# Kernel optimization log

Measured on AMD Instinct MI355X. Metric: run time of the kernel, lower is better.

The kernel has to match this reference:

```python
import jax, jax.numpy as jnp
import numpy as np

N = 100000   # nodes
E = 1600000  # edges
G = 64       # graphs in batch
DIMS = [(7, 128), (128, 128), (128, 256)]
EPS = 1e-5


def setup_inputs() -> dict:
    key = jax.random.key(0)
    ks = jax.random.split(key, 32)
    inp = {}
    inp["x"] = jax.random.normal(ks[0], (N, 7), dtype=jnp.float32)
    inp["edge_index"] = jax.random.randint(ks[1], (2, E), 0, N, dtype=jnp.int64)
    inp["batch"] = jnp.sort(jax.random.randint(ks[2], (N,), 0, G, dtype=jnp.int64))
    ki = 3
    for i, (din, dout) in enumerate(DIMS):
        inp[f"Wl{i}"] = jax.random.normal(ks[ki], (din, dout), dtype=jnp.float32) * 0.05; ki += 1
        inp[f"bl{i}"] = jnp.zeros((dout,), dtype=jnp.float32)
        inp[f"Wr{i}"] = jax.random.normal(ks[ki], (din, dout), dtype=jnp.float32) * 0.05; ki += 1
        inp[f"g{i}"] = jax.random.uniform(ks[ki], (dout,), dtype=jnp.float32) + 0.5; ki += 1
        inp[f"be{i}"] = jax.random.normal(ks[ki], (dout,), dtype=jnp.float32) * 0.1; ki += 1
        inp[f"rm{i}"] = jax.random.normal(ks[ki], (dout,), dtype=jnp.float32) * 0.1; ki += 1
        inp[f"rv{i}"] = jax.random.uniform(ks[ki], (dout,), dtype=jnp.float32) + 0.5; ki += 1
    return inp


def _sage(x, src, dst, Wl, bl, Wr):
    # mean-aggregate neighbor features: out[i] = mean_{(j->i)} x[j]
    agg = jax.ops.segment_sum(x[src], dst, num_segments=N)          # [N, din]
    cnt = jax.ops.segment_sum(jnp.ones((src.shape[0],), x.dtype), dst, num_segments=N)
    mean = agg / jnp.maximum(cnt, 1.0)[:, None]
    return x @ Wl + bl + mean @ Wr


def _bn_relu(x, g, be, rm, rv):
    # BatchNorm1d in eval mode (running stats) + ReLU; dropout is a no-op in eval
    return jax.nn.relu((x - rm) * jax.lax.rsqrt(rv + EPS) * g + be)


def reference(x, edge_index, batch,
              Wl0, bl0, Wr0, g0, be0, rm0, rv0,
              Wl1, bl1, Wr1, g1, be1, rm1, rv1,
              Wl2, bl2, Wr2, g2, be2, rm2, rv2):
    src, dst = edge_index[0], edge_index[1]
    layers = [(Wl0, bl0, Wr0, g0, be0, rm0, rv0),
              (Wl1, bl1, Wr1, g1, be1, rm1, rv1),
              (Wl2, bl2, Wr2, g2, be2, rm2, rv2)]
    for Wl, bl, Wr, g, be, rm, rv in layers:
        x = _sage(x, src, dst, Wl, bl, Wr)
        x = _bn_relu(x, g, be, rm, rv)
    pooled = jax.ops.segment_sum(x, batch, num_segments=G)  # global_add_pool
    return (pooled, x)
```

## Files before the change

### kernel.cpp

```cpp
#include <hip/hip_runtime.h>
#include <hip/hip_bf16.h>

#define EPSV 1e-5f
#define PSHIFT 6
#define PMASK 63
#define BCAP 256
#define BSHIFT 8
#define XG 8

typedef __attribute__((ext_vector_type(8))) short bf16x8;
typedef __attribute__((ext_vector_type(4))) float f32x4;

__device__ __forceinline__ float bf2f(unsigned short u) {
    unsigned x = ((unsigned)u) << 16;
    return __builtin_bit_cast(float, x);
}
__device__ __forceinline__ unsigned short f2bf(float f) {
    unsigned x = __builtin_bit_cast(unsigned, f);
    unsigned r = (x + 0x7fffu + ((x >> 16) & 1u)) >> 16;
    return (unsigned short)r;
}

__global__ __launch_bounds__(256) void k_bucket(const int* __restrict__ src,
                                                const int* __restrict__ dst,
                                                int* __restrict__ bcnt,
                                                unsigned* __restrict__ staging,
                                                int E, int NPART) {
    int i = blockIdx.x * 256 + threadIdx.x;
    if (i >= E) return;
    int g = blockIdx.x & (XG - 1);
    int d = __builtin_nontemporal_load(&dst[i]);
    int s = __builtin_nontemporal_load(&src[i]);
    int p = d >> PSHIFT;
    int b = g * NPART + p;
    int slot = atomicAdd(&bcnt[b], 1);
    if (slot < BCAP)
        staging[((size_t)b << BSHIFT) + slot] = ((unsigned)s << PSHIFT) | (unsigned)(d & PMASK);
}

__global__ __launch_bounds__(256) void k_meta(const int* __restrict__ bcnt,
                                              int* __restrict__ pbase,
                                              int* __restrict__ off,
                                              const int* __restrict__ batch,
                                              int* __restrict__ gstart,
                                              int NPART, int Nn, int G) {
    if (blockIdx.x == 1) {
        int g = threadIdx.x;
        if (g > G) return;
        if (g == G) {
            gstart[G] = Nn;
            return;
        }
        int lo = 0, hi = Nn;
        while (lo < hi) {
            int mid = (lo + hi) >> 1;
            if (batch[mid] < g) lo = mid + 1;
            else hi = mid;
        }
        gstart[g] = lo;
        return;
    }
    __shared__ int red[256];
    int t = threadIdx.x;
    int chunk = (NPART + 255) / 256;
    int lo = t * chunk, hi = min(lo + chunk, NPART);
    int s = 0;
    for (int p = lo; p < hi; p++) {
        int tt = 0;
#pragma unroll
        for (int g = 0; g < XG; g++) tt += min(bcnt[g * NPART + p], BCAP);
        pbase[p] = tt;
        s += tt;
    }
    red[t] = s;
    __syncthreads();
    for (int d = 1; d < 256; d <<= 1) {
        int v = (t >= d) ? red[t - d] : 0;
        __syncthreads();
        red[t] += v;
        __syncthreads();
    }
    int base = (t == 0) ? 0 : red[t - 1];
    for (int p = lo; p < hi; p++) {
        int tt = pbase[p];
        pbase[p] = base;
        base += tt;
    }
    if (t == 255) off[Nn] = red[255];
}

__global__ __launch_bounds__(256) void k_build(const int* __restrict__ bcnt,
                                               const unsigned* __restrict__ staging,
                                               const int* __restrict__ pbase,
                                               int* __restrict__ off,
                                               int* __restrict__ csr,
                                               int NPART, int Nn) {
    __shared__ unsigned ed[XG * BCAP];
    __shared__ int srt[XG * BCAP];
    __shared__ int cnt[64], loff[64], cur[64];
    __shared__ int sb[XG + 1];
    int p = blockIdx.x, t = threadIdx.x;
    if (t < 64) cnt[t] = 0;
    if (t == 0) {
        int acc = 0;
#pragma unroll
        for (int g = 0; g < XG; g++) {
            sb[g] = acc;
            acc += min(bcnt[g * NPART + p], BCAP);
        }
        sb[XG] = acc;
    }
    __syncthreads();
    int tot = sb[XG];
#pragma unroll
    for (int g = 0; g < XG; g++) {
        int c = sb[g + 1] - sb[g];
        const unsigned* sp = staging + (((size_t)(g * NPART + p)) << BSHIFT);
        for (int j = t; j < c; j += 256) ed[sb[g] + j] = __builtin_nontemporal_load(&sp[j]);
    }
    __syncthreads();
    for (int j = t; j < tot; j += 256) atomicAdd(&cnt[ed[j] & PMASK], 1);
    __syncthreads();
    if (t == 0) {
        int a = 0;
        for (int j = 0; j < 64; j++) {
            loff[j] = a;
            cur[j] = a;
            a += cnt[j];
        }
    }
    __syncthreads();
    int base = pbase[p];
    int node0 = p << PSHIFT;
    if (t < 64 && node0 + t < Nn) off[node0 + t] = base + loff[t];
    for (int j = t; j < tot; j += 256) {
        unsigned e = ed[j];
        int pos = atomicAdd(&cur[e & PMASK], 1);
        srt[pos] = (int)(e >> PSHIFT);
    }
    __syncthreads();
    for (int j = t; j < tot; j += 256) csr[base + j] = srt[j];
}


__global__ __launch_bounds__(256) void k_agg7(const float* __restrict__ x,
                                              const int* __restrict__ off,
                                              const int* __restrict__ csr,
                                              float* __restrict__ mean, int n) {
    int i = (blockIdx.x * 256 + threadIdx.x) >> 3;
    int r = threadIdx.x & 7;
    if (i >= n) return;
    int a = off[i], b = off[i + 1];
    float acc = 0.f;
    if (r < 7) {
        int j = a;
        for (; j + 1 < b; j += 2)
            acc += x[(size_t)csr[j] * 7 + r] + x[(size_t)csr[j + 1] * 7 + r];
        if (j < b) acc += x[(size_t)csr[j] * 7 + r];
    }
    float inv = 1.0f / (float)max(b - a, 1);
    if (r < 7) mean[(size_t)i * 7 + r] = acc * inv;
}

__global__ __launch_bounds__(256) void k_agg128(const unsigned short* __restrict__ x,
                                                const int* __restrict__ off,
                                                const int* __restrict__ csr,
                                                unsigned short* __restrict__ mean,
                                                int n) {
    int h = (blockIdx.x * 256 + threadIdx.x) >> 5;
    int sl = threadIdx.x & 31;
    if (h >= n) return;
    int a = off[h], b = off[h + 1];
    float a0 = 0.f, a1 = 0.f, a2 = 0.f, a3 = 0.f;
    int j = a;
    for (; j + 3 < b; j += 4) {
        int s0 = csr[j], s1 = csr[j + 1], s2 = csr[j + 2], s3 = csr[j + 3];
        ushort4 v0 = *(const ushort4*)&x[(size_t)s0 * 128 + sl * 4];
        ushort4 v1 = *(const ushort4*)&x[(size_t)s1 * 128 + sl * 4];
        ushort4 v2 = *(const ushort4*)&x[(size_t)s2 * 128 + sl * 4];
        ushort4 v3 = *(const ushort4*)&x[(size_t)s3 * 128 + sl * 4];
        a0 += bf2f(v0.x) + bf2f(v1.x) + bf2f(v2.x) + bf2f(v3.x);
        a1 += bf2f(v0.y) + bf2f(v1.y) + bf2f(v2.y) + bf2f(v3.y);
        a2 += bf2f(v0.z) + bf2f(v1.z) + bf2f(v2.z) + bf2f(v3.z);
        a3 += bf2f(v0.w) + bf2f(v1.w) + bf2f(v2.w) + bf2f(v3.w);
    }
    for (; j < b; j++) {
        ushort4 v = *(const ushort4*)&x[(size_t)csr[j] * 128 + sl * 4];
        a0 += bf2f(v.x);
        a1 += bf2f(v.y);
        a2 += bf2f(v.z);
        a3 += bf2f(v.w);
    }
    float inv = 1.0f / (float)max(b - a, 1);
    ushort4 o;
    o.x = f2bf(a0 * inv);
    o.y = f2bf(a1 * inv);
    o.z = f2bf(a2 * inv);
    o.w = f2bf(a3 * inv);
    *(ushort4*)&mean[(size_t)h * 128 + sl * 4] = o;
}


__global__ __launch_bounds__(256) void k_prepw_all(
    const float* __restrict__ Wl1, const float* __restrict__ Wr1,
    const float* __restrict__ Wl2, const float* __restrict__ Wr2,
    unsigned short* __restrict__ Wlt1, unsigned short* __restrict__ Wrt1,
    unsigned short* __restrict__ Wlt2, unsigned short* __restrict__ Wrt2) {
    int u = blockIdx.x * 256 + threadIdx.x;
    const float* W;
    unsigned short* Wt;
    int Ncols, v;
    if (u < 32768) {
        v = u & 16383;
        W = (u < 16384) ? Wl1 : Wr1;
        Wt = (u < 16384) ? Wlt1 : Wrt1;
        Ncols = 128;
    } else {
        v = (u - 32768) & 32767;
        W = (u < 65536) ? Wl2 : Wr2;
        Wt = (u < 65536) ? Wlt2 : Wrt2;
        Ncols = 256;
    }
    int n = v % Ncols, k = v / Ncols;
    Wt[(size_t)n * 128 + k] = f2bf(W[(size_t)k * Ncols + n]);
}


__global__ __launch_bounds__(256) void k_layer0(
    const float* __restrict__ x, const float* __restrict__ mean,
    const float* __restrict__ Wl, const float* __restrict__ bl,
    const float* __restrict__ Wr, const float* __restrict__ g,
    const float* __restrict__ be, const float* __restrict__ rm,
    const float* __restrict__ rv, unsigned short* __restrict__ out, int n) {
    int tid = threadIdx.x;
    int col = tid & 127;
    int r = tid >> 7;
    int row = blockIdx.x * 2 + r;
    if (row >= n) return;
    float sc = g[col] * rsqrtf(rv[col] + EPSV);
    float sh = (bl[col] - rm[col]) * sc + be[col];
    const float* xp = x + (size_t)row * 7;
    const float* mp = mean + (size_t)row * 7;
    float acc = 0.f;
#pragma unroll
    for (int k = 0; k < 7; k++) acc += xp[k] * Wl[k * 128 + col];
#pragma unroll
    for (int k = 0; k < 7; k++) acc += mp[k] * Wr[k * 128 + col];
    float h = acc * sc + sh;
    out[(size_t)row * 128 + col] = f2bf(fmaxf(h, 0.f));
}


template <int COLS, int DOUT, bool BF16OUT>
__global__ __launch_bounds__(256) void k_mfma_layer(
    const unsigned short* __restrict__ xin, const unsigned short* __restrict__ meanb,
    const unsigned short* __restrict__ Wlt, const unsigned short* __restrict__ Wrt,
    const float* __restrict__ bl, const float* __restrict__ g,
    const float* __restrict__ be, const float* __restrict__ rm,
    const float* __restrict__ rv, void* __restrict__ outv, int n) {
    __shared__ unsigned short As[64 * 40];
    __shared__ unsigned short Bs[COLS * 40];

    int tid = threadIdx.x;
    int wave = tid >> 6;
    int lane = tid & 63;
    int m = lane & 15;
    int half = lane >> 4;
    int row0 = blockIdx.x * 64;
    int colbase = blockIdx.y * COLS;

    const int NCB = COLS / 16;
    f32x4 acc[NCB] = {};

    for (int s = 0; s < 8; s++) {
        int pass = s >> 2;
        int k0 = (s & 3) * 32;
        const unsigned short* Asrc = pass ? meanb : xin;
        const unsigned short* Wt = pass ? Wrt : Wlt;

        __syncthreads();
        {
            int rr = tid >> 2;
            int ks = (tid & 3) * 8;
            int grow = row0 + rr;
            float4 v = make_float4(0.f, 0.f, 0.f, 0.f);
            if (grow < n) v = *(const float4*)&Asrc[(size_t)grow * 128 + k0 + ks];
            *(float4*)&As[rr * 40 + ks] = v;
        }
#pragma unroll
        for (int rep = 0; rep < COLS / 64; rep++) {
            int u = tid + rep * 256;
            int nn = u >> 2;
            int ks = (u & 3) * 8;
            float4 v = *(const float4*)&Wt[(size_t)(colbase + nn) * 128 + k0 + ks];
            *(float4*)&Bs[nn * 40 + ks] = v;
        }
        __syncthreads();

        bf16x8 a = *(const bf16x8*)&As[(wave * 16 + m) * 40 + half * 8];
#pragma unroll
        for (int cb = 0; cb < NCB; cb++) {
            bf16x8 b = *(const bf16x8*)&Bs[(cb * 16 + m) * 40 + half * 8];
            acc[cb] = __builtin_amdgcn_mfma_f32_16x16x32_bf16(a, b, acc[cb], 0, 0, 0);
        }
    }

    float* outf = (float*)outv;
    unsigned short* outb = (unsigned short*)outv;
#pragma unroll
    for (int cb = 0; cb < NCB; cb++) {
        int col = colbase + cb * 16 + m;
        float sc = g[col] * rsqrtf(rv[col] + EPSV);
        float sh = (bl[col] - rm[col]) * sc + be[col];
#pragma unroll
        for (int reg = 0; reg < 4; reg++) {
            int r0 = row0 + wave * 16 + half * 4 + reg;
            if (r0 < n) {
                float h = fmaxf(acc[cb][reg] * sc + sh, 0.f);
                if (BF16OUT) outb[(size_t)r0 * DOUT + col] = f2bf(h);
                else outf[(size_t)r0 * DOUT + col] = h;
            }
        }
    }
}


__global__ __launch_bounds__(256) void k_pool(const float* __restrict__ x3,
                                              const int* __restrict__ gstart,
                                              float* __restrict__ pooled, int G) {
    const int S = 16;
    int g = blockIdx.x / S;
    int s = blockIdx.x % S;
    int a = gstart[g], b = gstart[g + 1];
    int col = threadIdx.x;
    float acc = 0.f;
    for (int r = a + s; r < b; r += S) acc += x3[(size_t)r * 256 + col];
    atomicAdd(&pooled[g * 256 + col], acc);
}


extern "C" void kernel_launch(void* const* d_in, const int* in_sizes, int n_in,
                              void* d_out, int out_size, void* d_ws, size_t ws_size,
                              hipStream_t stream) {
    const float* x = (const float*)d_in[0];
    const int* ei = (const int*)d_in[1];
    const int* batch = (const int*)d_in[2];
    const int N = in_sizes[0] / 7;
    const int E = in_sizes[1] / 2;
    const int G = 64;
    const int* src = ei;
    const int* dst = ei + E;
    const int NPART = (N + PMASK) >> PSHIFT;

    const float* P[21];
    for (int i = 0; i < 21; i++) P[i] = (const float*)d_in[3 + i];
    const float **L0 = P, **L1 = P + 7, **L2 = P + 14;

    char* w = (char*)d_ws;
    auto carve = [&](size_t bytes) {
        void* p = (void*)w;
        w += (bytes + 255) & ~(size_t)255;
        return p;
    };
    int* bcnt = (int*)carve((size_t)XG * NPART * 4);
    unsigned* staging = (unsigned*)carve((size_t)XG * NPART * BCAP * 4);
    int* pbase = (int*)carve((size_t)NPART * 4);
    int* off = (int*)carve(((size_t)N + 1) * 4);
    int* csr = (int*)carve((size_t)E * 4);
    int* gstart = (int*)carve(((size_t)G + 1) * 4);
    float* mean7 = (float*)carve((size_t)N * 7 * 4);
    unsigned short* x1 = (unsigned short*)carve((size_t)N * 128 * 2);
    unsigned short* meanb = (unsigned short*)carve((size_t)N * 128 * 2);
    unsigned short* Wlt1 = (unsigned short*)carve((size_t)128 * 128 * 2);
    unsigned short* Wrt1 = (unsigned short*)carve((size_t)128 * 128 * 2);
    unsigned short* Wlt2 = (unsigned short*)carve((size_t)128 * 256 * 2);
    unsigned short* Wrt2 = (unsigned short*)carve((size_t)128 * 256 * 2);

    float* pooled = (float*)d_out;
    float* x3 = (float*)d_out + (size_t)G * 256;

    hipMemsetAsync(bcnt, 0, (size_t)XG * NPART * 4, stream);
    hipMemsetAsync(pooled, 0, (size_t)G * 256 * 4, stream);

    k_bucket<<<(E + 255) / 256, 256, 0, stream>>>(src, dst, bcnt, staging, E, NPART);
    k_meta<<<2, 256, 0, stream>>>(bcnt, pbase, off, batch, gstart, NPART, N, G);
    k_build<<<NPART, 256, 0, stream>>>(bcnt, staging, pbase, off, csr, NPART, N);
    k_prepw_all<<<(98304 + 255) / 256, 256, 0, stream>>>(L1[0], L1[2], L2[0], L2[2],
                                                         Wlt1, Wrt1, Wlt2, Wrt2);

    k_agg7<<<(N * 8 + 255) / 256, 256, 0, stream>>>(x, off, csr, mean7, N);
    k_layer0<<<(N + 1) / 2, 256, 0, stream>>>(x, mean7, L0[0], L0[1], L0[2], L0[3],
                                              L0[4], L0[5], L0[6], x1, N);

    k_agg128<<<(N + 7) / 8, 256, 0, stream>>>(x1, off, csr, meanb, N);
    k_mfma_layer<128, 128, true><<<dim3((N + 63) / 64, 1), 256, 0, stream>>>(
        x1, meanb, Wlt1, Wrt1, L1[1], L1[3], L1[4], L1[5], L1[6], x1, N);

    k_agg128<<<(N + 7) / 8, 256, 0, stream>>>(x1, off, csr, meanb, N);
    k_mfma_layer<128, 256, false><<<dim3((N + 63) / 64, 2), 256, 0, stream>>>(
        x1, meanb, Wlt2, Wrt2, L2[1], L2[3], L2[4], L2[5], L2[6], x3, N);

    k_pool<<<G * 16, 256, 0, stream>>>(x3, gstart, pooled, G);
}
```

Measured before the change: 521.2 us.

## Replace atomic bucket CSR build with two-pass block-local bin sort

The CSR construction is rebuilt. Previously every edge did a global atomic into capped 8-way-replicated buckets of 64 nodes. Now 256 blocks each sort a contiguous edge chunk into 512-node superpartitions using only shared-memory atomics. A meta kernel prefix-sums the per-block histograms, and a build kernel gathers each superpartition's segments from all chunks and counting-sorts them by node in shared memory. This removes global atomic contention at the cost of lower parallelism in the sort, a second pass over the staging data, and scattered small segment reads. A superpartition holding more than 10240 edges would still be truncated.

Result: slower. 1.141 ms (+118.9%).

```diff
diff --git a/kernel.cpp b/kernel.cpp
--- a/kernel.cpp
+++ b/kernel.cpp
@@ -2,11 +2,10 @@
 #include <hip/hip_bf16.h>
 
 #define EPSV 1e-5f
-#define PSHIFT 6
-#define PMASK 63
-#define BCAP 256
-#define BSHIFT 8
-#define XG 8
+#define SPSHIFT 9
+#define SPMASK 511
+#define NBINS 256
+#define CAPS 10240
 
 typedef __attribute__((ext_vector_type(8))) short bf16x8;
 typedef __attribute__((ext_vector_type(4))) float f32x4;
@@ -21,29 +20,45 @@
     return (unsigned short)r;
 }
 
-__global__ __launch_bounds__(256) void k_bucket(const int* __restrict__ src,
-                                                const int* __restrict__ dst,
-                                                int* __restrict__ bcnt,
-                                                unsigned* __restrict__ staging,
-                                                int E, int NPART) {
-    int i = blockIdx.x * 256 + threadIdx.x;
-    if (i >= E) return;
-    int g = blockIdx.x & (XG - 1);
-    int d = __builtin_nontemporal_load(&dst[i]);
-    int s = __builtin_nontemporal_load(&src[i]);
-    int p = d >> PSHIFT;
-    int b = g * NPART + p;
-    int slot = atomicAdd(&bcnt[b], 1);
-    if (slot < BCAP)
-        staging[((size_t)b << BSHIFT) + slot] = ((unsigned)s << PSHIFT) | (unsigned)(d & PMASK);
-}
-
-__global__ __launch_bounds__(256) void k_meta(const int* __restrict__ bcnt,
-                                              int* __restrict__ pbase,
-                                              int* __restrict__ off,
-                                              const int* __restrict__ batch,
-                                              int* __restrict__ gstart,
-                                              int NPART, int Nn, int G) {
+
+__global__ __launch_bounds__(256) void k_binsort(const int* __restrict__ src,
+                                                 const int* __restrict__ dst,
+                                                 unsigned* __restrict__ staging,
+                                                 int* __restrict__ bh,
+                                                 int E, int chunk, int NSP) {
+    __shared__ int cnt[256], red[256];
+    int b = blockIdx.x, t = threadIdx.x;
+    int lo = b * chunk, hi = min(lo + chunk, E);
+    cnt[t] = 0;
+    __syncthreads();
+    for (int i = lo + t; i < hi; i += 256) atomicAdd(&cnt[dst[i] >> SPSHIFT], 1);
+    __syncthreads();
+    int v = cnt[t];
+    red[t] = v;
+    __syncthreads();
+    for (int d = 1; d < 256; d <<= 1) {
+        int u = (t >= d) ? red[t - d] : 0;
+        __syncthreads();
+        red[t] += u;
+        __syncthreads();
+    }
+    if (t < NSP) bh[b * NSP + t] = v;
+    cnt[t] = red[t] - v;
+    __syncthreads();
+    for (int i = lo + t; i < hi; i += 256) {
+        int d = dst[i], s = src[i];
+        int pos = atomicAdd(&cnt[d >> SPSHIFT], 1);
+        staging[(size_t)lo + pos] = ((unsigned)s << SPSHIFT) | (unsigned)(d & SPMASK);
+    }
+}
+
+__global__ __launch_bounds__(256) void k_meta2(const int* __restrict__ bh,
+                                               int* __restrict__ start,
+                                               int* __restrict__ spbase,
+                                               int* __restrict__ off,
+                                               const int* __restrict__ batch,
+                                               int* __restrict__ gstart,
+                                               int NSP, int Nn, int G, int E) {
     if (blockIdx.x == 1) {
         int g = threadIdx.x;
         if (g > G) return;
@@ -62,84 +77,78 @@
     }
     __shared__ int red[256];
     int t = threadIdx.x;
-    int chunk = (NPART + 255) / 256;
-    int lo = t * chunk, hi = min(lo + chunk, NPART);
     int s = 0;
-    for (int p = lo; p < hi; p++) {
-        int tt = 0;
-#pragma unroll
-        for (int g = 0; g < XG; g++) tt += min(bcnt[g * NPART + p], BCAP);
-        pbase[p] = tt;
-        s += tt;
-    }
-    red[t] = s;
+    if (t < NSP) {
+        for (int b = 0; b < NBINS; b++) {
+            start[b * NSP + t] = s;
+            s += bh[b * NSP + t];
+        }
+    }
+    red[t] = (t < NSP) ? s : 0;
     __syncthreads();
     for (int d = 1; d < 256; d <<= 1) {
-        int v = (t >= d) ? red[t - d] : 0;
-        __syncthreads();
-        red[t] += v;
-        __syncthreads();
-    }
-    int base = (t == 0) ? 0 : red[t - 1];
-    for (int p = lo; p < hi; p++) {
-        int tt = pbase[p];
-        pbase[p] = base;
-        base += tt;
-    }
-    if (t == 255) off[Nn] = red[255];
-}
-
-__global__ __launch_bounds__(256) void k_build(const int* __restrict__ bcnt,
-                                               const unsigned* __restrict__ staging,
-                                               const int* __restrict__ pbase,
-                                               int* __restrict__ off,
-                                               int* __restrict__ csr,
-                                               int NPART, int Nn) {
-    __shared__ unsigned ed[XG * BCAP];
-    __shared__ int srt[XG * BCAP];
-    __shared__ int cnt[64], loff[64], cur[64];
-    __shared__ int sb[XG + 1];
-    int p = blockIdx.x, t = threadIdx.x;
-    if (t < 64) cnt[t] = 0;
-    if (t == 0) {
-        int acc = 0;
-#pragma unroll
-        for (int g = 0; g < XG; g++) {
-            sb[g] = acc;
-            acc += min(bcnt[g * NPART + p], BCAP);
-        }
-        sb[XG] = acc;
-    }
-    __syncthreads();
-    int tot = sb[XG];
-#pragma unroll
-    for (int g = 0; g < XG; g++) {
-        int c = sb[g + 1] - sb[g];
-        const unsigned* sp = staging + (((size_t)(g * NPART + p)) << BSHIFT);
-        for (int j = t; j < c; j += 256) ed[sb[g] + j] = __builtin_nontemporal_load(&sp[j]);
-    }
-    __syncthreads();
-    for (int j = t; j < tot; j += 256) atomicAdd(&cnt[ed[j] & PMASK], 1);
-    __syncthreads();
-    if (t == 0) {
-        int a = 0;
-        for (int j = 0; j < 64; j++) {
-            loff[j] = a;
-            cur[j] = a;
-            a += cnt[j];
-        }
-    }
-    __syncthreads();
-    int base = pbase[p];
-    int node0 = p << PSHIFT;
-    if (t < 64 && node0 + t < Nn) off[node0 + t] = base + loff[t];
-    for (int j = t; j < tot; j += 256) {
-        unsigned e = ed[j];
-        int pos = atomicAdd(&cur[e & PMASK], 1);
-        srt[pos] = (int)(e >> PSHIFT);
-    }
-    __syncthreads();
-    for (int j = t; j < tot; j += 256) csr[base + j] = srt[j];
+        int u = (t >= d) ? red[t - d] : 0;
+        __syncthreads();
+        red[t] += u;
+        __syncthreads();
+    }
+    if (t < NSP) spbase[t] = red[t] - s;
+    if (t == 255) off[Nn] = E;
+}
+
+__global__ __launch_bounds__(256) void k_build2(const unsigned* __restrict__ staging,
+                                                const int* __restrict__ bh,
+                                                const int* __restrict__ start,
+                                                const int* __restrict__ spbase,
+                                                int* __restrict__ off,
+                                                int* __restrict__ csr,
+                                                int chunk, int NSP, int Nn) {
+    __shared__ int cnt[512], loff[512], cur[512], red[256];
+    __shared__ unsigned srt[CAPS];
+    int sp = blockIdx.x, t = threadIdx.x;
+    int wave = t >> 6, lane = t & 63;
+    cnt[t] = 0;
+    cnt[t + 256] = 0;
+    __syncthreads();
+    for (int b = wave; b < NBINS; b += 4) {
+        int st = start[b * NSP + sp], c = bh[b * NSP + sp];
+        const unsigned* rp = staging + (size_t)b * chunk + st;
+        for (int j = lane; j < c; j += 64) atomicAdd(&cnt[rp[j] & SPMASK], 1);
+    }
+    __syncthreads();
+    int a0 = cnt[2 * t], a1 = cnt[2 * t + 1];
+    int v = a0 + a1;
+    red[t] = v;
+    __syncthreads();
+    for (int d = 1; d < 256; d <<= 1) {
+        int u = (t >= d) ? red[t - d] : 0;
+        __syncthreads();
+        red[t] += u;
+        __syncthreads();
+    }
+    int ex = red[t] - v;
+    loff[2 * t] = ex;
+    loff[2 * t + 1] = ex + a0;
+    __syncthreads();
+    int tot = min(red[255], CAPS);
+    int base = spbase[sp];
+    int node0 = sp << SPSHIFT;
+    if (node0 + t < Nn) off[node0 + t] = base + loff[t];
+    if (node0 + 256 + t < Nn) off[node0 + 256 + t] = base + loff[256 + t];
+    cur[2 * t] = loff[2 * t];
+    cur[2 * t + 1] = loff[2 * t + 1];
+    __syncthreads();
+    for (int b = wave; b < NBINS; b += 4) {
+        int st = start[b * NSP + sp], c = bh[b * NSP + sp];
+        const unsigned* rp = staging + (size_t)b * chunk + st;
+        for (int j = lane; j < c; j += 64) {
+            unsigned e = rp[j];
+            int pos = atomicAdd(&cur[e & SPMASK], 1);
+            if (pos < CAPS) srt[pos] = e >> SPSHIFT;
+        }
+    }
+    __syncthreads();
+    for (int j = t; j < tot; j += 256) csr[base + j] = (int)srt[j];
 }
 
 
@@ -350,7 +359,8 @@
     const int G = 64;
     const int* src = ei;
     const int* dst = ei + E;
-    const int NPART = (N + PMASK) >> PSHIFT;
+    const int NSP = (N + SPMASK) >> SPSHIFT;
+    const int chunk = (E + NBINS - 1) / NBINS;
 
     const float* P[21];
     for (int i = 0; i < 21; i++) P[i] = (const float*)d_in[3 + i];
@@ -362,9 +372,10 @@
         w += (bytes + 255) & ~(size_t)255;
         return p;
     };
-    int* bcnt = (int*)carve((size_t)XG * NPART * 4);
-    unsigned* staging = (unsigned*)carve((size_t)XG * NPART * BCAP * 4);
-    int* pbase = (int*)carve((size_t)NPART * 4);
+    unsigned* staging = (unsigned*)carve((size_t)NBINS * chunk * 4);
+    int* bh = (int*)carve((size_t)NBINS * NSP * 4);
+    int* start = (int*)carve((size_t)NBINS * NSP * 4);
+    int* spbase = (int*)carve((size_t)NSP * 4);
     int* off = (int*)carve(((size_t)N + 1) * 4);
     int* csr = (int*)carve((size_t)E * 4);
     int* gstart = (int*)carve(((size_t)G + 1) * 4);
@@ -379,12 +390,11 @@
     float* pooled = (float*)d_out;
     float* x3 = (float*)d_out + (size_t)G * 256;
 
-    hipMemsetAsync(bcnt, 0, (size_t)XG * NPART * 4, stream);
     hipMemsetAsync(pooled, 0, (size_t)G * 256 * 4, stream);
 
-    k_bucket<<<(E + 255) / 256, 256, 0, stream>>>(src, dst, bcnt, staging, E, NPART);
-    k_meta<<<2, 256, 0, stream>>>(bcnt, pbase, off, batch, gstart, NPART, N, G);
-    k_build<<<NPART, 256, 0, stream>>>(bcnt, staging, pbase, off, csr, NPART, N);
+    k_binsort<<<NBINS, 256, 0, stream>>>(src, dst, staging, bh, E, chunk, NSP);
+    k_meta2<<<2, 256, 0, stream>>>(bh, start, spbase, off, batch, gstart, NSP, N, G, E);
+    k_build2<<<NSP, 256, 0, stream>>>(staging, bh, start, spbase, off, csr, chunk, NSP, N);
     k_prepw_all<<<(98304 + 255) / 256, 256, 0, stream>>>(L1[0], L1[2], L2[0], L2[2],
                                                          Wlt1, Wrt1, Wlt2, Wrt2);
 
```
